# Kernel tuning notes

Measured on AMD Instinct MI355X. Metric: run time of the kernel, lower is better.

The kernel has to match this reference:

```python
import jax, jax.numpy as jnp
import numpy as np

EMBED = 1024
HEADS = 16
HEAD_DIM = EMBED // HEADS
SCALE = HEAD_DIM ** -0.5


def setup_inputs() -> dict:
    key = jax.random.key(0)
    ks = jax.random.split(key, 9)
    init = lambda k, shape: jax.random.normal(k, shape, dtype=jnp.float32) * 0.02
    return {
        "hidden_states": jax.random.normal(ks[0], (32, 257, EMBED), dtype=jnp.float32),
        "Wq": init(ks[1], (EMBED, EMBED)), "bq": init(ks[2], (EMBED,)),
        "Wk": init(ks[3], (EMBED, EMBED)), "bk": init(ks[4], (EMBED,)),
        "Wv": init(ks[5], (EMBED, EMBED)), "bv": init(ks[6], (EMBED,)),
        "Wo": init(ks[7], (EMBED, EMBED)), "bo": init(ks[8], (EMBED,)),
    }


def reference(hidden_states, Wq, bq, Wk, bk, Wv, bv, Wo, bo):
    b, t, d = hidden_states.shape
    # projections (torch Linear: x @ W.T + b); scale applied to Q
    q = (hidden_states @ Wq.T + bq) * SCALE
    k = hidden_states @ Wk.T + bk
    v = hidden_states @ Wv.T + bv
    # [b, h, t, hd]
    q = q.reshape(b, t, HEADS, HEAD_DIM).transpose(0, 2, 1, 3)
    k = k.reshape(b, t, HEADS, HEAD_DIM).transpose(0, 2, 1, 3)
    v = v.reshape(b, t, HEADS, HEAD_DIM).transpose(0, 2, 1, 3)
    # attention scores + softmax (dropout p is a no-op in eval mode)
    scores = jnp.einsum("bhqd,bhkd->bhqk", q, k)
    probs = jax.nn.softmax(scores, axis=-1)
    ctx = jnp.einsum("bhqk,bhkd->bhqd", probs, v)
    ctx = ctx.transpose(0, 2, 1, 3).reshape(b, t, d)
    return ctx @ Wo.T + bo
```

## Files before the change

### kernel.cpp

```cpp
#include <hip/hip_runtime.h>


#define B_   32
#define T_   257
#define TP   272
#define H_   16
#define HD_  64
#define D_   1024
#define NTOK 8224
#define BH_  512
#define FRAG_PER_BH 17408

typedef __bf16 bf16;
typedef __bf16 bf16x4 __attribute__((ext_vector_type(4)));
typedef __bf16 bf16x8 __attribute__((ext_vector_type(8)));
typedef short  s16x4  __attribute__((ext_vector_type(4)));
typedef float  floatx4 __attribute__((ext_vector_type(4)));

static constexpr size_t SZ_XB   = (size_t)NTOK * D_ * 2;
static constexpr size_t SZ_WQKV = (size_t)3 * D_ * D_ * 2;
static constexpr size_t SZ_W    = (size_t)D_ * D_ * 2;
static constexpr size_t SZ_QK   = (size_t)BH_ * FRAG_PER_BH * 2;
static constexpr size_t SZ_CTX  = (size_t)NTOK * D_ * 2;

static constexpr size_t OFF_XB   = 0;
static constexpr size_t OFF_WQKV = OFF_XB + SZ_XB;
static constexpr size_t OFF_WO   = OFF_WQKV + SZ_WQKV;
static constexpr size_t OFF_Q    = OFF_WO + SZ_W;
static constexpr size_t OFF_K    = OFF_Q + SZ_QK;
static constexpr size_t OFF_V    = OFF_K + SZ_QK;
static constexpr size_t OFF_CTX  = OFF_V + SZ_QK;

#define GLD16(gp, lp)                                                        \
  __builtin_amdgcn_global_load_lds(                                          \
      (const __attribute__((address_space(1))) void*)(gp),                   \
      (__attribute__((address_space(3))) void*)(lp), 16, 0, 0)

__global__ void cast_bf16_kernel(const float* __restrict__ src,
                                 bf16* __restrict__ dst, int n4) {
  int i = blockIdx.x * blockDim.x + threadIdx.x;
  int stride = gridDim.x * blockDim.x;
  for (int idx = i; idx < n4; idx += stride) {
    float4 v = reinterpret_cast<const float4*>(src)[idx];
    bf16x4 o;
    o[0] = (bf16)v.x; o[1] = (bf16)v.y; o[2] = (bf16)v.z; o[3] = (bf16)v.w;
    reinterpret_cast<bf16x4*>(dst)[idx] = o;
  }
}

__global__ void cast4_kernel(const float* __restrict__ s0, const float* __restrict__ s1,
                             const float* __restrict__ s2, const float* __restrict__ s3,
                             bf16* __restrict__ d0, bf16* __restrict__ d1,
                             bf16* __restrict__ d2, bf16* __restrict__ d3, int n4) {
  const float* s = (blockIdx.y == 0) ? s0 : (blockIdx.y == 1) ? s1
                   : (blockIdx.y == 2) ? s2 : s3;
  bf16* d = (blockIdx.y == 0) ? d0 : (blockIdx.y == 1) ? d1
            : (blockIdx.y == 2) ? d2 : d3;
  int i = blockIdx.x * blockDim.x + threadIdx.x;
  int stride = gridDim.x * blockDim.x;
  for (int idx = i; idx < n4; idx += stride) {
    float4 v = reinterpret_cast<const float4*>(s)[idx];
    bf16x4 o;
    o[0] = (bf16)v.x; o[1] = (bf16)v.y; o[2] = (bf16)v.z; o[3] = (bf16)v.w;
    reinterpret_cast<bf16x4*>(d)[idx] = o;
  }
}

__device__ __forceinline__ int qk_frag_idx(int t, int d) {
  return ((t >> 4) * 8 + (d >> 3)) * 128 + (t & 15) * 8 + (d & 7);
}
__device__ __forceinline__ int v_frag_idx(int t, int d) {
  return ((t >> 4) * 4 + (d >> 4)) * 256 + ((t >> 2) & 3) * 64 + (d & 15) * 4 + (t & 3);
}

__global__ __launch_bounds__(256) void qkv_gemm(
    const bf16* __restrict__ xb, const bf16* __restrict__ wqkv,
    const float* __restrict__ bq, const float* __restrict__ bk,
    const float* __restrict__ bv,
    bf16* __restrict__ Qf, bf16* __restrict__ Kf, bf16* __restrict__ Vf) {
  __shared__ bf16 Ash[128 * 32];
  __shared__ bf16 Bsh[128 * 32];

  const int linear = blockIdx.x;
  const int nbg = ((linear & 7) * 3 + ((linear >> 3) % 3)) * 128;
  const int mbase = (linear / 24) * 128;
  const int tid = threadIdx.x;
  const int lane = tid & 63;
  const int w = tid >> 6;
  const int wr = w >> 1, wc = w & 1;
  const int n15 = lane & 15, quad = lane >> 4;

  const int lrow = lane >> 2;
  const int lseg = (lane & 3) * 8;

  floatx4 acc[4][4] = {};

  for (int k0 = 0; k0 < D_; k0 += 32) {
#pragma unroll
    for (int c = 0; c < 2; c++) {
      int r0 = w * 32 + c * 16;
      int row = r0 + lrow;
      int gm = mbase + row; if (gm > NTOK - 1) gm = NTOK - 1;
      GLD16(xb + (size_t)gm * D_ + k0 + lseg, Ash + r0 * 32);
      GLD16(wqkv + (size_t)(nbg + row) * D_ + k0 + lseg, Bsh + r0 * 32);
    }
    __syncthreads();
    bf16x8 af[4], bfr[4];
#pragma unroll
    for (int i = 0; i < 4; i++) {
      af[i]  = *reinterpret_cast<const bf16x8*>(Ash + (wr * 64 + i * 16 + n15) * 32 + quad * 8);
      bfr[i] = *reinterpret_cast<const bf16x8*>(Bsh + (wc * 64 + i * 16 + n15) * 32 + quad * 8);
    }
#pragma unroll
    for (int i = 0; i < 4; i++)
#pragma unroll
      for (int j = 0; j < 4; j++)
        acc[i][j] = __builtin_amdgcn_mfma_f32_16x16x32_bf16(af[i], bfr[j], acc[i][j], 0, 0, 0);
    __syncthreads();
  }

#pragma unroll
  for (int i = 0; i < 4; i++) {
    int rowb = mbase + wr * 64 + i * 16 + quad * 4;
#pragma unroll
    for (int j = 0; j < 4; j++) {
      int nc = nbg + wc * 64 + j * 16 + n15;
      int z = nc >> 10;
      int col = nc & 1023;
      float bval = (z == 0) ? bq[col] : (z == 1) ? bk[col] : bv[col];
      float scale = (z == 0) ? 0.125f : 1.0f;
      int h = col >> 6, hd = col & 63;
#pragma unroll
      for (int r = 0; r < 4; r++) {
        int m = rowb + r;
        if (m < NTOK) {
          float v = (acc[i][j][r] + bval) * scale;
          int b = m / T_;
          int t = m - b * T_;
          size_t base = (size_t)(b * H_ + h) * FRAG_PER_BH;
          if (z == 2)
            Vf[base + v_frag_idx(t, hd)] = (bf16)v;
          else {
            bf16* dst = (z == 0) ? Qf : Kf;
            dst[base + qk_frag_idx(t, hd)] = (bf16)v;
          }
        }
      }
    }
  }
}

__global__ __launch_bounds__(256) void attn_kernel(
    const bf16* __restrict__ Qf, const bf16* __restrict__ Kf,
    const bf16* __restrict__ Vf, bf16* __restrict__ ctx) {
  const int bh = blockIdx.x;
  const int tid = threadIdx.x;
  const int lane = tid & 63, w = tid >> 6;
  const int n15 = lane & 15, quad = lane >> 4;
  const int b = bh >> 4, h = bh & 15;

  const bf16* Qb = Qf + (size_t)bh * FRAG_PER_BH;
  const bf16* Kb = Kf + (size_t)bh * FRAG_PER_BH;
  const bf16* Vb = Vf + (size_t)bh * FRAG_PER_BH;
  const int fo = quad * 128 + n15 * 8;
  const int vo = quad * 64 + n15 * 4;

  for (int qt = w; qt < 17; qt += 4) {
    bf16x8 qb0 = *reinterpret_cast<const bf16x8*>(Qb + qt * 1024 + fo);
    bf16x8 qb1 = *reinterpret_cast<const bf16x8*>(Qb + qt * 1024 + 512 + fo);

    floatx4 s[17];
#pragma unroll
    for (int kt = 0; kt < 17; kt++) {
      bf16x8 ka0 = *reinterpret_cast<const bf16x8*>(Kb + kt * 1024 + fo);
      bf16x8 ka1 = *reinterpret_cast<const bf16x8*>(Kb + kt * 1024 + 512 + fo);
      floatx4 c = {};
      c = __builtin_amdgcn_mfma_f32_16x16x32_bf16(ka0, qb0, c, 0, 0, 0);
      c = __builtin_amdgcn_mfma_f32_16x16x32_bf16(ka1, qb1, c, 0, 0, 0);
      s[kt] = c;
    }
    s[16][1] = -1e30f; s[16][2] = -1e30f; s[16][3] = -1e30f;
    if (quad != 0) s[16][0] = -1e30f;

    float m0 = -1e30f;
#pragma unroll
    for (int kt = 0; kt < 17; kt++)
#pragma unroll
      for (int r = 0; r < 4; r++) m0 = fmaxf(m0, s[kt][r]);
    m0 = fmaxf(m0, __shfl_xor(m0, 16));
    m0 = fmaxf(m0, __shfl_xor(m0, 32));

    float sum = 0.f;
    s16x4 pb[17];
#pragma unroll
    for (int kt = 0; kt < 17; kt++) {
      bf16x4 ph;
#pragma unroll
      for (int r = 0; r < 4; r++) {
        float p = __expf(s[kt][r] - m0);
        sum += p;
        ph[r] = (bf16)p;
      }
      pb[kt] = __builtin_bit_cast(s16x4, ph);
    }
    sum += __shfl_xor(sum, 16);
    sum += __shfl_xor(sum, 32);

    floatx4 o[4] = {};
#pragma unroll
    for (int kt = 0; kt < 17; kt++) {
#pragma unroll
      for (int dt = 0; dt < 4; dt++) {
        s16x4 va = *reinterpret_cast<const s16x4*>(Vb + (kt * 4 + dt) * 256 + vo);
        o[dt] = __builtin_amdgcn_mfma_f32_16x16x16bf16_1k(va, pb[kt], o[dt], 0, 0, 0);
      }
    }

    int q = qt * 16 + n15;
    if (q < T_) {
      float inv = 1.0f / sum;
      size_t ob = ((size_t)(b * T_ + q)) * D_ + h * 64 + quad * 4;
#pragma unroll
      for (int dt = 0; dt < 4; dt++) {
        bf16x4 ov;
#pragma unroll
        for (int r = 0; r < 4; r++) ov[r] = (bf16)(o[dt][r] * inv);
        *reinterpret_cast<bf16x4*>(ctx + ob + dt * 16) = ov;
      }
    }
  }
}

__global__ __launch_bounds__(256) void o_gemm(
    const bf16* __restrict__ ctx, const bf16* __restrict__ wo,
    const float* __restrict__ bo, float* __restrict__ out) {
  __shared__ bf16 Ash[128 * 32];
  __shared__ bf16 Bsh[128 * 32];

  const int linear = blockIdx.x;
  const int nbase = (linear & 7) * 128;
  const int mbase = (linear >> 3) * 128;
  const int tid = threadIdx.x;
  const int lane = tid & 63;
  const int w = tid >> 6;
  const int wr = w >> 1, wc = w & 1;
  const int n15 = lane & 15, quad = lane >> 4;

  const int lrow = lane >> 2;
  const int lseg = (lane & 3) * 8;

  floatx4 acc[4][4] = {};

  for (int k0 = 0; k0 < D_; k0 += 32) {
#pragma unroll
    for (int c = 0; c < 2; c++) {
      int r0 = w * 32 + c * 16;
      int row = r0 + lrow;
      int gm = mbase + row; if (gm > NTOK - 1) gm = NTOK - 1;
      GLD16(ctx + (size_t)gm * D_ + k0 + lseg, Ash + r0 * 32);
      GLD16(wo + (size_t)(nbase + row) * D_ + k0 + lseg, Bsh + r0 * 32);
    }
    __syncthreads();
    bf16x8 af[4], bfr[4];
#pragma unroll
    for (int i = 0; i < 4; i++) {
      af[i]  = *reinterpret_cast<const bf16x8*>(Ash + (wr * 64 + i * 16 + n15) * 32 + quad * 8);
      bfr[i] = *reinterpret_cast<const bf16x8*>(Bsh + (wc * 64 + i * 16 + n15) * 32 + quad * 8);
    }
#pragma unroll
    for (int i = 0; i < 4; i++)
#pragma unroll
      for (int j = 0; j < 4; j++)
        acc[i][j] = __builtin_amdgcn_mfma_f32_16x16x32_bf16(af[i], bfr[j], acc[i][j], 0, 0, 0);
    __syncthreads();
  }

#pragma unroll
  for (int i = 0; i < 4; i++) {
    int rowb = mbase + wr * 64 + i * 16 + quad * 4;
#pragma unroll
    for (int j = 0; j < 4; j++) {
      int col = nbase + wc * 64 + j * 16 + n15;
      float bval = bo[col];
#pragma unroll
      for (int r = 0; r < 4; r++) {
        int m = rowb + r;
        if (m < NTOK) out[(size_t)m * D_ + col] = acc[i][j][r] + bval;
      }
    }
  }
}

extern "C" void kernel_launch(void* const* d_in, const int* in_sizes, int n_in,
                              void* d_out, int out_size, void* d_ws, size_t ws_size,
                              hipStream_t stream) {
  const float* hs = (const float*)d_in[0];
  const float* Wq = (const float*)d_in[1];
  const float* bq = (const float*)d_in[2];
  const float* Wk = (const float*)d_in[3];
  const float* bk = (const float*)d_in[4];
  const float* Wv = (const float*)d_in[5];
  const float* bv = (const float*)d_in[6];
  const float* Wo = (const float*)d_in[7];
  const float* bo = (const float*)d_in[8];

  char* ws = (char*)d_ws;
  bf16* xb   = (bf16*)(ws + OFF_XB);
  bf16* wqkv = (bf16*)(ws + OFF_WQKV);
  bf16* wob  = (bf16*)(ws + OFF_WO);
  bf16* Qfw  = (bf16*)(ws + OFF_Q);
  bf16* Kfw  = (bf16*)(ws + OFF_K);
  bf16* Vfw  = (bf16*)(ws + OFF_V);
  bf16* ctx  = (bf16*)(ws + OFF_CTX);

  cast_bf16_kernel<<<2048, 256, 0, stream>>>(hs, xb, NTOK * D_ / 4);
  cast4_kernel<<<dim3(256, 4), 256, 0, stream>>>(
      Wq, Wk, Wv, Wo,
      wqkv, wqkv + (size_t)D_ * D_, wqkv + (size_t)2 * D_ * D_, wob,
      D_ * D_ / 4);

  qkv_gemm<<<1560, 256, 0, stream>>>(xb, wqkv, bq, bk, bv, Qfw, Kfw, Vfw);
  attn_kernel<<<BH_, 256, 0, stream>>>(Qfw, Kfw, Vfw, ctx);
  o_gemm<<<520, 256, 0, stream>>>(ctx, wob, bo, (float*)d_out);
}
```

Measured before the change: 270.1 us.

## Stage QKV epilogue through LDS for vector stores; cache K/V in LDS

The QKV GEMM epilogue now writes the biased, scaled tile into shared memory and then emits 16-byte vector stores into the fragment layouts, replacing scattered per-element global stores. The V fragment layout changes so that one 16-byte load feeds two MFMAs. The attention kernel loads the whole K and V block for each batch-head into LDS with async global-to-LDS copies, so the four waves share one copy instead of each rereading from global. The cost is about 68KB of LDS per attention block, which limits occupancy, and more complex epilogue indexing that has to handle tiles crossing a batch boundary.

Measured after the change: 252.1 us. 6.7% less time.

```diff
diff --git a/kernel.cpp b/kernel.cpp
--- a/kernel.cpp
+++ b/kernel.cpp
@@ -15,13 +15,13 @@
 typedef __bf16 bf16x4 __attribute__((ext_vector_type(4)));
 typedef __bf16 bf16x8 __attribute__((ext_vector_type(8)));
 typedef short  s16x4  __attribute__((ext_vector_type(4)));
+typedef short  s16x8  __attribute__((ext_vector_type(8)));
 typedef float  floatx4 __attribute__((ext_vector_type(4)));
 
 static constexpr size_t SZ_XB   = (size_t)NTOK * D_ * 2;
 static constexpr size_t SZ_WQKV = (size_t)3 * D_ * D_ * 2;
 static constexpr size_t SZ_W    = (size_t)D_ * D_ * 2;
 static constexpr size_t SZ_QK   = (size_t)BH_ * FRAG_PER_BH * 2;
-static constexpr size_t SZ_CTX  = (size_t)NTOK * D_ * 2;
 
 static constexpr size_t OFF_XB   = 0;
 static constexpr size_t OFF_WQKV = OFF_XB + SZ_XB;
@@ -66,20 +66,15 @@
   }
 }
 
-__device__ __forceinline__ int qk_frag_idx(int t, int d) {
-  return ((t >> 4) * 8 + (d >> 3)) * 128 + (t & 15) * 8 + (d & 7);
-}
-__device__ __forceinline__ int v_frag_idx(int t, int d) {
-  return ((t >> 4) * 4 + (d >> 4)) * 256 + ((t >> 2) & 3) * 64 + (d & 15) * 4 + (t & 3);
-}
 
 __global__ __launch_bounds__(256) void qkv_gemm(
     const bf16* __restrict__ xb, const bf16* __restrict__ wqkv,
     const float* __restrict__ bq, const float* __restrict__ bk,
     const float* __restrict__ bv,
     bf16* __restrict__ Qf, bf16* __restrict__ Kf, bf16* __restrict__ Vf) {
-  __shared__ bf16 Ash[128 * 32];
-  __shared__ bf16 Bsh[128 * 32];
+  __shared__ bf16 smem[9216];
+  bf16* Ash = smem;
+  bf16* Bsh = smem + 4096;
 
   const int linear = blockIdx.x;
   const int nbg = ((linear & 7) * 3 + ((linear >> 3) % 3)) * 128;
@@ -119,40 +114,101 @@
     __syncthreads();
   }
 
-#pragma unroll
-  for (int i = 0; i < 4; i++) {
-    int rowb = mbase + wr * 64 + i * 16 + quad * 4;
-#pragma unroll
-    for (int j = 0; j < 4; j++) {
-      int nc = nbg + wc * 64 + j * 16 + n15;
-      int z = nc >> 10;
-      int col = nc & 1023;
-      float bval = (z == 0) ? bq[col] : (z == 1) ? bk[col] : bv[col];
-      float scale = (z == 0) ? 0.125f : 1.0f;
-      int h = col >> 6, hd = col & 63;
-#pragma unroll
-      for (int r = 0; r < 4; r++) {
-        int m = rowb + r;
-        if (m < NTOK) {
-          float v = (acc[i][j][r] + bval) * scale;
-          int b = m / T_;
-          int t = m - b * T_;
-          size_t base = (size_t)(b * H_ + h) * FRAG_PER_BH;
-          if (z == 2)
-            Vf[base + v_frag_idx(t, hd)] = (bf16)v;
-          else {
-            bf16* dst = (z == 0) ? Qf : Kf;
-            dst[base + qk_frag_idx(t, hd)] = (bf16)v;
+  const int z = nbg >> 10;
+  bf16* zdst = (z == 0) ? Qf : (z == 1) ? Kf : Vf;
+  const float scale = (z == 0) ? 0.125f : 1.0f;
+  const float* bias = (z == 0) ? bq : (z == 1) ? bk : bv;
+  const int zoff = nbg & 1023;
+
+  const int bA = mbase / T_;
+  const int tA = mbase - bA * T_;
+  const int tEndA = (tA + 128 < T_) ? tA + 128 : T_;
+  const int tgA0 = tA >> 4;
+  const int nA = ((tEndA - 1) >> 4) - tgA0 + 1;
+  int nU = nA, tEndB = 0;
+  if (tA + 128 > T_ && bA + 1 < B_) {
+    tEndB = tA + 128 - T_;
+    nU += ((tEndB - 1) >> 4) + 1;
+  }
+
+  for (int half = 0; half < 2; half++) {
+    if (wc == half) {
+#pragma unroll
+      for (int i = 0; i < 4; i++)
+#pragma unroll
+        for (int j = 0; j < 4; j++) {
+          int colL = j * 16 + n15;
+          float bval = bias[zoff + half * 64 + colL];
+#pragma unroll
+          for (int r = 0; r < 4; r++) {
+            int rowL = wr * 64 + i * 16 + quad * 4 + r;
+            smem[rowL * 72 + colL] = (bf16)((acc[i][j][r] + bval) * scale);
           }
         }
-      }
-    }
+    }
+    __syncthreads();
+    const int h = (zoff >> 6) + half;
+    for (int u = w; u < nU; u += 4) {
+      int b, tg, tlo, thi;
+      if (u < nA) {
+        b = bA; tg = tgA0 + u;
+        tlo = (tA > tg * 16) ? tA : tg * 16;
+        int te = tg * 16 + 16; thi = (te < tEndA) ? te : tEndA;
+      } else {
+        b = bA + 1; tg = u - nA;
+        tlo = tg * 16;
+        int te = tg * 16 + 16; thi = (te < tEndB) ? te : tEndB;
+      }
+      bf16* gb = zdst + (size_t)(b * H_ + h) * FRAG_PER_BH + tg * 1024;
+      if (z != 2) {
+        int ki = lane & 15, dc = lane >> 4;
+        int t = tg * 16 + ki;
+        if (t >= tlo && t < thi) {
+          int rowL = b * T_ + t - mbase;
+          bf16x8 v0 = *reinterpret_cast<const bf16x8*>(smem + rowL * 72 + dc * 8);
+          bf16x8 v1 = *reinterpret_cast<const bf16x8*>(smem + rowL * 72 + 32 + dc * 8);
+          *reinterpret_cast<bf16x8*>(gb + dc * 128 + ki * 8) = v0;
+          *reinterpret_cast<bf16x8*>(gb + 512 + dc * 128 + ki * 8) = v1;
+        }
+      } else {
+        int q2 = (lane >> 4) & 3, d16 = lane & 15;
+        int tb = tg * 16 + q2 * 4;
+        bool full = (tb >= tlo) && (tb + 3 < thi);
+#pragma unroll
+        for (int p = 0; p < 2; p++) {
+          bf16x8 vv;
+#pragma unroll
+          for (int dp = 0; dp < 2; dp++)
+#pragma unroll
+            for (int ki = 0; ki < 4; ki++) {
+              int t = tb + ki;
+              int rr = (b * T_ + t - mbase) & 127;
+              vv[dp * 4 + ki] = smem[rr * 72 + p * 32 + dp * 16 + d16];
+            }
+          bf16* cp = gb + (p * 4 + q2) * 128 + d16 * 8;
+          if (full) {
+            *reinterpret_cast<bf16x8*>(cp) = vv;
+          } else {
+#pragma unroll
+            for (int dp = 0; dp < 2; dp++)
+#pragma unroll
+              for (int ki = 0; ki < 4; ki++) {
+                int t = tb + ki;
+                if (t >= tlo && t < thi) cp[dp * 4 + ki] = vv[dp * 4 + ki];
+              }
+          }
+        }
+      }
+    }
+    __syncthreads();
   }
 }
 
 __global__ __launch_bounds__(256) void attn_kernel(
     const bf16* __restrict__ Qf, const bf16* __restrict__ Kf,
     const bf16* __restrict__ Vf, bf16* __restrict__ ctx) {
+  __shared__ bf16 smem[34816];
+
   const int bh = blockIdx.x;
   const int tid = threadIdx.x;
   const int lane = tid & 63, w = tid >> 6;
@@ -162,8 +218,18 @@
   const bf16* Qb = Qf + (size_t)bh * FRAG_PER_BH;
   const bf16* Kb = Kf + (size_t)bh * FRAG_PER_BH;
   const bf16* Vb = Vf + (size_t)bh * FRAG_PER_BH;
+
+#pragma unroll
+  for (int j = 0; j < 17; j++) {
+    int c = w * 17 + j;
+    const bf16* src = (c < 34) ? (Kb + c * 512) : (Vb + (c - 34) * 512);
+    GLD16(src + lane * 8, smem + c * 512);
+  }
+  __syncthreads();
+  const bf16* Ksh = smem;
+  const bf16* Vsh = smem + 17408;
+
   const int fo = quad * 128 + n15 * 8;
-  const int vo = quad * 64 + n15 * 4;
 
   for (int qt = w; qt < 17; qt += 4) {
     bf16x8 qb0 = *reinterpret_cast<const bf16x8*>(Qb + qt * 1024 + fo);
@@ -172,8 +238,8 @@
     floatx4 s[17];
 #pragma unroll
     for (int kt = 0; kt < 17; kt++) {
-      bf16x8 ka0 = *reinterpret_cast<const bf16x8*>(Kb + kt * 1024 + fo);
-      bf16x8 ka1 = *reinterpret_cast<const bf16x8*>(Kb + kt * 1024 + 512 + fo);
+      bf16x8 ka0 = *reinterpret_cast<const bf16x8*>(Ksh + kt * 1024 + fo);
+      bf16x8 ka1 = *reinterpret_cast<const bf16x8*>(Ksh + kt * 1024 + 512 + fo);
       floatx4 c = {};
       c = __builtin_amdgcn_mfma_f32_16x16x32_bf16(ka0, qb0, c, 0, 0, 0);
       c = __builtin_amdgcn_mfma_f32_16x16x32_bf16(ka1, qb1, c, 0, 0, 0);
@@ -210,9 +276,14 @@
 #pragma unroll
     for (int kt = 0; kt < 17; kt++) {
 #pragma unroll
-      for (int dt = 0; dt < 4; dt++) {
-        s16x4 va = *reinterpret_cast<const s16x4*>(Vb + (kt * 4 + dt) * 256 + vo);
-        o[dt] = __builtin_amdgcn_mfma_f32_16x16x16bf16_1k(va, pb[kt], o[dt], 0, 0, 0);
+      for (int p = 0; p < 2; p++) {
+        bf16x8 vv = *reinterpret_cast<const bf16x8*>(
+            Vsh + ((kt * 2 + p) * 4 + quad) * 128 + n15 * 8);
+        s16x8 v16 = __builtin_bit_cast(s16x8, vv);
+        s16x4 vlo = __builtin_shufflevector(v16, v16, 0, 1, 2, 3);
+        s16x4 vhi = __builtin_shufflevector(v16, v16, 4, 5, 6, 7);
+        o[p * 2]     = __builtin_amdgcn_mfma_f32_16x16x16bf16_1k(vlo, pb[kt], o[p * 2], 0, 0, 0);
+        o[p * 2 + 1] = __builtin_amdgcn_mfma_f32_16x16x16bf16_1k(vhi, pb[kt], o[p * 2 + 1], 0, 0, 0);
       }
     }
 
```
